# Kernel optimization log

Hardware: AMD Instinct MI355X
Metric: run time of the kernel (lower is better)

## Reference

```python
import jax, jax.numpy as jnp
import numpy as np

B, N, D = 2, 2048, 1024
H, DH = 16, 64
EPS = 1e-5


def _layernorm(t, g, b):
    m = jnp.mean(t, axis=-1, keepdims=True)
    v = jnp.mean(jnp.square(t - m), axis=-1, keepdims=True)
    return (t - m) * jax.lax.rsqrt(v + EPS) * g + b


def setup_inputs() -> dict:
    key = jax.random.key(0)
    ks = jax.random.split(key, 4)
    return {
        "x": jax.random.normal(ks[0], (B, N, D), dtype=jnp.float32),
        "ln_g": jnp.ones((D,), jnp.float32),
        "ln_b": jnp.zeros((D,), jnp.float32),
        "lnc_g": jnp.ones((D,), jnp.float32),
        "lnc_b": jnp.zeros((D,), jnp.float32),
        "Wq": jax.random.normal(ks[1], (D, H * DH), jnp.float32) * 0.02,
        "Wkv": jax.random.normal(ks[2], (D, 2 * H * DH), jnp.float32) * 0.02,
        "Wo": jax.random.normal(ks[3], (H * DH, D), jnp.float32) * 0.02,
    }


def reference(x, ln_g, ln_b, lnc_g, lnc_b, Wq, Wkv, Wo):
    scale = DH ** (-0.5)
    xn = _layernorm(x, ln_g, ln_b)          # self-attn: context = x
    cn = _layernorm(x, lnc_g, lnc_b)
    q = xn @ Wq                              # [b, n, h*d]
    kv = cn @ Wkv
    k, v = jnp.split(kv, 2, axis=-1)
    # b n (h d) -> b h n d
    q = q.reshape(B, N, H, DH).transpose(0, 2, 1, 3)
    k = k.reshape(B, N, H, DH).transpose(0, 2, 1, 3)
    v = v.reshape(B, N, H, DH).transpose(0, 2, 1, 3)
    sim = jnp.einsum("bhnd,bhmd->bhnm", q, k) * scale
    neg = -jnp.finfo(sim.dtype).max
    causal = jnp.tril(jnp.ones((N, N), dtype=bool))  # allow j <= i
    sim = jnp.where(causal[None, None], sim, neg)
    attn = jax.nn.softmax(sim.astype(jnp.float32), axis=-1)
    out = jnp.einsum("bhnm,bhmd->bhnd", attn, v)
    out = out.transpose(0, 2, 1, 3).reshape(B, N, H * DH)
    return out @ Wo
```

## Files before the change

### kernel.cpp

```cpp
#include <hip/hip_runtime.h>
#include <hip/hip_bf16.h>

#define B_  2
#define N_  2048
#define D_  1024
#define H_  16
#define DH_ 64
#define BN_ROWS (B_ * N_)
#define EPS_ 1e-5f
#define QKV_N 3072

typedef __attribute__((ext_vector_type(8))) short bf16x8_t;
typedef __attribute__((ext_vector_type(4))) short bf16x4_t;
typedef __attribute__((ext_vector_type(4))) float f32x4_t;

#define MFMA16(a, b, c) __builtin_amdgcn_mfma_f32_16x16x16bf16_1k(a, b, c, 0, 0, 0)

typedef const unsigned int __attribute__((address_space(1)))* gas_ptr;
typedef unsigned int __attribute__((address_space(3)))* las_ptr;

__device__ __forceinline__ void async16(const unsigned short* g, unsigned short* l) {
    __builtin_amdgcn_global_load_lds((gas_ptr)g, (las_ptr)l, 16, 0, 0);
}

__device__ __forceinline__ unsigned short f2bf(float f) {
    unsigned int u = __float_as_uint(f);
    unsigned int r = u + 0x7FFFu + ((u >> 16) & 1u);
    return (unsigned short)(r >> 16);
}

__device__ __forceinline__ unsigned int pk2bf(float a, float b) {
    __hip_bfloat162 t = __float22bfloat162_rn(float2{a, b});
    return *(unsigned int*)&t;
}

__global__ __launch_bounds__(256) void ln_wt_kernel(
    const float* __restrict__ x,
    const float* __restrict__ g1, const float* __restrict__ b1,
    const float* __restrict__ g2, const float* __restrict__ b2,
    const float* __restrict__ Wq, const float* __restrict__ Wkv,
    const float* __restrict__ Wo,
    unsigned short* __restrict__ xn, unsigned short* __restrict__ cn,
    unsigned short* __restrict__ wqkvT, unsigned short* __restrict__ woT) {
    const int bid = blockIdx.x;
    const int tid = threadIdx.x;

    if (bid < BN_ROWS) {
        const int row = bid;
        const float4 v = ((const float4*)(x + (size_t)row * D_))[tid];

        float s  = v.x + v.y + v.z + v.w;
        float s2 = v.x * v.x + v.y * v.y + v.z * v.z + v.w * v.w;
        #pragma unroll
        for (int off = 32; off > 0; off >>= 1) {
            s  += __shfl_down(s,  off);
            s2 += __shfl_down(s2, off);
        }
        __shared__ float red[8];
        if ((tid & 63) == 0) { red[tid >> 6] = s; red[4 + (tid >> 6)] = s2; }
        __syncthreads();
        const float S  = red[0] + red[1] + red[2] + red[3];
        const float S2 = red[4] + red[5] + red[6] + red[7];
        const float mean = S * (1.0f / D_);
        const float var  = S2 * (1.0f / D_) - mean * mean;
        const float rstd = rsqrtf(var + EPS_);

        const float4 G1 = ((const float4*)g1)[tid];
        const float4 B1 = ((const float4*)b1)[tid];
        const float4 G2 = ((const float4*)g2)[tid];
        const float4 B2 = ((const float4*)b2)[tid];

        float nx[4] = { (v.x - mean) * rstd, (v.y - mean) * rstd,
                        (v.z - mean) * rstd, (v.w - mean) * rstd };
        ushort4 o1, o2;
        o1.x = f2bf(nx[0] * G1.x + B1.x); o1.y = f2bf(nx[1] * G1.y + B1.y);
        o1.z = f2bf(nx[2] * G1.z + B1.z); o1.w = f2bf(nx[3] * G1.w + B1.w);
        o2.x = f2bf(nx[0] * G2.x + B2.x); o2.y = f2bf(nx[1] * G2.y + B2.y);
        o2.z = f2bf(nx[2] * G2.z + B2.z); o2.w = f2bf(nx[3] * G2.w + B2.w);
        ((ushort4*)(xn + (size_t)row * D_))[tid] = o1;
        ((ushort4*)(cn + (size_t)row * D_))[tid] = o2;
    } else {
        const int zz = bid - BN_ROWS;
        const float* src;
        unsigned short* dst;
        int N, t;
        if (zz < 1024)      { src = Wq;  dst = wqkvT;                       N = 1024; t = zz; }
        else if (zz < 3072) { src = Wkv; dst = wqkvT + (size_t)1024 * 1024; N = 2048; t = zz - 1024; }
        else                { src = Wo;  dst = woT;                         N = 1024; t = zz - 3072; }
        const int nb = N / 32;
        const int n0 = (t % nb) * 32, k0 = (t / nb) * 32;

        __shared__ float tile[32][33];
        const int tx = tid & 31, ty = tid >> 5;
        #pragma unroll
        for (int i = 0; i < 4; i++)
            tile[ty + i * 8][tx] = src[(size_t)(k0 + ty + i * 8) * N + n0 + tx];
        __syncthreads();
        #pragma unroll
        for (int i = 0; i < 4; i++)
            dst[(size_t)(n0 + ty + i * 8) * 1024 + k0 + tx] = f2bf(tile[tx][ty + i * 8]);
    }
}

template <int BM, bool FUSED, bool BF16OUT, int MINW>
__global__ __launch_bounds__(256, MINW) void gemm_kernel(
    const unsigned short* __restrict__ A0, const unsigned short* __restrict__ A1,
    const unsigned short* __restrict__ Bt, void* __restrict__ Cv,
    unsigned short* __restrict__ vt, int M, int N, int K) {
    constexpr int WM = BM / 2, MT = WM / 16, AI = BM / 32;
    __shared__ unsigned short As[BM * 64];
    __shared__ unsigned short Bs[128 * 64];
    const int tid = threadIdx.x, lane = tid & 63, w = tid >> 6;
    const int quad = lane >> 4, l16 = lane & 15;
    const int lr8 = lane >> 3, pg8 = lane & 7;
    const int wr = (w >> 1) * WM, wc = (w & 1) * 64;
    const int bm = blockIdx.y * BM, bn = blockIdx.x * 128;
    const unsigned short* A = (FUSED && bn >= 1024) ? A1 : A0;
    const float cscale = (FUSED && bn < 1024) ? 0.180336880111120f : 1.0f;

    f32x4_t acc[MT][4] = {};
    for (int k0 = 0; k0 < K; k0 += 64) {
        #pragma unroll
        for (int i = 0; i < AI; i++) {
            const int rb = w * (BM / 4) + i * 8;
            const int r  = rb + lr8;
            const int g  = pg8 ^ (r & 7);
            async16(&A[(size_t)(bm + r) * K + k0 + g * 8], &As[rb * 64]);
        }
        #pragma unroll
        for (int i = 0; i < 4; i++) {
            const int rb = w * 32 + i * 8;
            const int r  = rb + lr8;
            const int g  = pg8 ^ (r & 7);
            async16(&Bt[(size_t)(bn + r) * K + k0 + g * 8], &Bs[rb * 64]);
        }
        __syncthreads();
        #pragma unroll
        for (int kk = 0; kk < 64; kk += 32) {
            bf16x8_t af[MT], bfr[4];
            const int g0 = (kk >> 3) + quad;
            #pragma unroll
            for (int t = 0; t < MT; t++)
                af[t] = *(const bf16x8_t*)&As[(wr + t * 16 + l16) * 64 +
                                              ((g0 ^ (l16 & 7)) * 8)];
            #pragma unroll
            for (int t = 0; t < 4; t++)
                bfr[t] = *(const bf16x8_t*)&Bs[(wc + t * 16 + l16) * 64 +
                                               ((g0 ^ (l16 & 7)) * 8)];
            #pragma unroll
            for (int mt = 0; mt < MT; mt++)
                #pragma unroll
                for (int nt = 0; nt < 4; nt++)
                    acc[mt][nt] = __builtin_amdgcn_mfma_f32_16x16x32_bf16(
                        af[mt], bfr[nt], acc[mt][nt], 0, 0, 0);
        }
        __syncthreads();
    }

    if (FUSED && bn >= 2048) {
        const int seq0 = bm + wr;
        const int bq = seq0 >> 11;
        const int kt = (seq0 & (N_ - 1)) >> 6;
        #pragma unroll
        for (int nt = 0; nt < 4; nt++) {
            const int c = (bn - 2048) + wc + nt * 16 + l16;
            unsigned short* dst =
                vt + (((size_t)(bq * 32 + kt) * 1024) + c) * 64;
            #pragma unroll
            for (int mt = 0; mt < 4; mt++) {
                uint2 v2 = { pk2bf(acc[mt][nt][0], acc[mt][nt][1]),
                             pk2bf(acc[mt][nt][2], acc[mt][nt][3]) };
                *(uint2*)&dst[mt * 16 + quad * 4] = v2;
            }
        }
        return;
    }

    #pragma unroll
    for (int mt = 0; mt < MT; mt++)
        #pragma unroll
        for (int nt = 0; nt < 4; nt++)
            #pragma unroll
            for (int r = 0; r < 4; r++) {
                const int row = bm + wr + mt * 16 + quad * 4 + r;
                const int col = bn + wc + nt * 16 + l16;
                if (BF16OUT)
                    ((unsigned short*)Cv)[(size_t)row * N + col] =
                        f2bf(acc[mt][nt][r] * cscale);
                else
                    ((float*)Cv)[(size_t)row * N + col] = acc[mt][nt][r];
            }
}

__global__ __launch_bounds__(512, 4) void flash_attn_kernel(
    const unsigned short* __restrict__ qkv, const unsigned short* __restrict__ vt,
    unsigned short* __restrict__ out) {
    __shared__ unsigned short Qs[64 * 64];
    __shared__ unsigned short Ks[2][64 * 64];
    __shared__ unsigned short Vts[3][64 * 64];

    const int tid = threadIdx.x, lane = tid & 63, w = tid >> 6;
    const int quad = lane >> 4, l16 = lane & 15;
    const int lr8 = lane >> 3, pg8 = lane & 7;
    const int wq = w & 3;
    const int wk = w >> 2;
    const int bid = blockIdx.x;
    const int bh   = (bid & 7) * 4 + ((bid >> 3) & 3);
    const int pair = bid >> 5;
    const int b = bh >> 4, h = bh & 15;

    const unsigned short* qb  = qkv + (size_t)(b * N_) * QKV_N + h * DH_;
    const unsigned short* kb  = qb + 1024;
    const unsigned short* vtb = vt + ((size_t)(b * 32) * 1024 + h * 64) * 64;

    bf16x4_t ones4;
    #pragma unroll
    for (int j = 0; j < 4; j++) ones4[j] = (short)0x3F80;

    for (int phase = 0; phase < 2; phase++) {
        const int qt = phase ? (31 - pair) : pair;
        const int qs = qt * 64;
        const int niter = qt + 1;

        __syncthreads();

        f32x4_t o[4] = {};
        f32x4_t lacc = {};
        bf16x8_t qf[2];
        bf16x4_t pf[2];

        auto prefetch = [&](int t) {
            const int ksel = t & 1, vsel = t % 3;
            const int rb = w * 8;
            const int r  = rb + lr8;
            const int g  = pg8 ^ (r & 7);
            async16(&kb[(size_t)(t * 64 + r) * QKV_N + g * 8], &Ks[ksel][rb * 64]);
            async16(&vtb[((size_t)t * 1024 + r) * 64 + g * 8], &Vts[vsel][rb * 64]);
        };
        auto do_qk = [&](int kbuf, f32x4_t* s) {
            #pragma unroll
            for (int k2 = 0; k2 < 2; k2++) {
                const int g0 = k2 * 4 + quad;
                #pragma unroll
                for (int kt = 0; kt < 2; kt++) {
                    const int ktg = wk * 2 + kt;
                    const bf16x8_t a = *(const bf16x8_t*)&Ks[kbuf][
                        (ktg * 16 + l16) * 64 + (g0 ^ (l16 & 7)) * 8];
                    s[kt] = __builtin_amdgcn_mfma_f32_16x16x32_bf16(
                        a, qf[k2], s[kt], 0, 0, 0);
                }
            }
        };
        auto do_exp = [&](const f32x4_t* s, int js, bool edge) {
            #pragma unroll
            for (int kt = 0; kt < 2; kt++) {
                const int ktg = wk * 2 + kt;
                float p[4];
                #pragma unroll
                for (int r = 0; r < 4; r++) {
                    float sv = s[kt][r];
                    if (edge) {
                        const int key = js + ktg * 16 + quad * 4 + r;
                        const int qy  = qs + wq * 16 + l16;
                        if (key > qy) sv = -3e38f;
                    }
                    p[r] = __builtin_amdgcn_exp2f(sv);
                }
                uint2 pk = { pk2bf(p[0], p[1]), pk2bf(p[2], p[3]) };
                pf[kt] = *(bf16x4_t*)&pk;
            }
        };
        auto do_pv = [&](int vbuf) {
            #pragma unroll
            for (int kt = 0; kt < 2; kt++) {
                const int ktg = wk * 2 + kt;
                const int g = ktg * 2 + (quad >> 1);
                const int col = ((g ^ (l16 & 7)) * 8) + (quad & 1) * 4;
                #pragma unroll
                for (int nt = 0; nt < 4; nt++) {
                    const bf16x4_t bv = *(const bf16x4_t*)&Vts[vbuf][
                        (nt * 16 + l16) * 64 + col];
                    o[nt] = MFMA16(pf[kt], bv, o[nt]);
                }
                lacc = MFMA16(pf[kt], ones4, lacc);
            }
        };

        {
            const int rb = w * 8;
            const int r  = rb + lr8;
            const int g  = pg8 ^ (r & 7);
            async16(&qb[(size_t)(qs + r) * QKV_N + g * 8], &Qs[rb * 64]);
        }
        prefetch(0);
        __syncthreads();

        if (niter > 1) prefetch(1);
        #pragma unroll
        for (int k2 = 0; k2 < 2; k2++) {
            const int g0 = k2 * 4 + quad;
            qf[k2] = *(const bf16x8_t*)&Qs[
                (wq * 16 + l16) * 64 + (g0 ^ (l16 & 7)) * 8];
        }
        {
            f32x4_t s[2] = {};
            do_qk(0, s);
            do_exp(s, 0, niter == 1);
        }

        for (int jt = 1; jt < niter; jt++) {
            __syncthreads();
            if (jt + 1 < niter) prefetch(jt + 1);
            f32x4_t s[2] = {};
            do_qk(jt & 1, s);
            do_pv((jt - 1) % 3);
            do_exp(s, jt * 64, jt == niter - 1);
        }
        do_pv((niter - 1) % 3);

        __syncthreads();
        float* red = (float*)&Vts[0][0];
        if (wk == 1) {
            #pragma unroll
            for (int r = 0; r < 4; r++) {
                const int q = quad * 4 + r;
                const int base = (wq * 16 + q) * 68;
                #pragma unroll
                for (int nt = 0; nt < 4; nt++)
                    red[base + nt * 16 + l16] = o[nt][r];
                red[base + 64] = lacc[r];
            }
        }
        __syncthreads();
        if (wk == 0) {
            #pragma unroll
            for (int r = 0; r < 4; r++) {
                const int q = quad * 4 + r;
                const int base = (wq * 16 + q) * 68;
                #pragma unroll
                for (int nt = 0; nt < 4; nt++)
                    o[nt][r] += red[base + nt * 16 + l16];
                const float inv = 1.0f / (lacc[r] + red[base + 64]);
                const int query = qs + wq * 16 + quad * 4 + r;
                const int row = b * N_ + query;
                #pragma unroll
                for (int nt = 0; nt < 4; nt++) {
                    const int col = h * DH_ + nt * 16 + l16;
                    out[(size_t)row * (H_ * DH_) + col] = f2bf(o[nt][r] * inv);
                }
            }
        }
    }
}

extern "C" void kernel_launch(void* const* d_in, const int* in_sizes, int n_in,
                              void* d_out, int out_size, void* d_ws, size_t ws_size,
                              hipStream_t stream) {
    const float* x     = (const float*)d_in[0];
    const float* ln_g  = (const float*)d_in[1];
    const float* ln_b  = (const float*)d_in[2];
    const float* lnc_g = (const float*)d_in[3];
    const float* lnc_b = (const float*)d_in[4];
    const float* Wq    = (const float*)d_in[5];
    const float* Wkv   = (const float*)d_in[6];
    const float* Wo    = (const float*)d_in[7];

    char* ws = (char*)d_ws;
    const size_t MB = 1024 * 1024;
    unsigned short* qkv   = (unsigned short*)(ws + 0 * MB);
    unsigned short* vtbuf = (unsigned short*)(ws + 24 * MB);
    unsigned short* xn    = (unsigned short*)(ws + 32 * MB);
    unsigned short* cn    = (unsigned short*)(ws + 40 * MB);
    unsigned short* wqkvT = (unsigned short*)(ws + 48 * MB);
    unsigned short* woT   = (unsigned short*)(ws + 54 * MB);
    unsigned short* ao    = xn;

    ln_wt_kernel<<<8192, 256, 0, stream>>>(
        x, ln_g, ln_b, lnc_g, lnc_b, Wq, Wkv, Wo, xn, cn, wqkvT, woT);

    gemm_kernel<128, true, true, 3>
        <<<dim3(QKV_N / 128, BN_ROWS / 128), 256, 0, stream>>>(
        xn, cn, wqkvT, qkv, vtbuf, BN_ROWS, QKV_N, D_);

    flash_attn_kernel<<<B_ * H_ * 16, 512, 0, stream>>>(qkv, vtbuf, ao);

    gemm_kernel<64, false, false, 2>
        <<<dim3(D_ / 128, BN_ROWS / 64), 256, 0, stream>>>(
        ao, nullptr, woT, (float*)d_out, nullptr, BN_ROWS, D_, H_ * DH_);
}
```

Measured before the change: 175.7 us.

## Load Q and K fragments directly to registers and repartition attention warps

The flash attention kernel no longer stages Q and K through LDS. Each wave loads its Q fragments (two 16-row tiles) and a 16-key slice of K straight from global memory into registers, double-buffered across iterations, while V is still staged asynchronously in LDS. Work is split so each wave owns one 16-key slice and 32 query rows, and the four partial accumulators are merged by a two-level LDS tree reduction. This cuts LDS traffic and capacity, but adds uncoalesced global loads for K, more accumulator registers, and extra barriers in the epilogue.

```diff
diff --git a/kernel.cpp b/kernel.cpp
--- a/kernel.cpp
+++ b/kernel.cpp
@@ -15,6 +15,7 @@
 typedef __attribute__((ext_vector_type(4))) float f32x4_t;
 
 #define MFMA16(a, b, c) __builtin_amdgcn_mfma_f32_16x16x16bf16_1k(a, b, c, 0, 0, 0)
+#define MFMA32(a, b, c) __builtin_amdgcn_mfma_f32_16x16x32_bf16(a, b, c, 0, 0, 0)
 
 typedef const unsigned int __attribute__((address_space(1)))* gas_ptr;
 typedef unsigned int __attribute__((address_space(3)))* las_ptr;
@@ -151,8 +152,7 @@
             for (int mt = 0; mt < MT; mt++)
                 #pragma unroll
                 for (int nt = 0; nt < 4; nt++)
-                    acc[mt][nt] = __builtin_amdgcn_mfma_f32_16x16x32_bf16(
-                        af[mt], bfr[nt], acc[mt][nt], 0, 0, 0);
+                    acc[mt][nt] = MFMA32(af[mt], bfr[nt], acc[mt][nt]);
         }
         __syncthreads();
     }
@@ -195,15 +195,14 @@
 __global__ __launch_bounds__(512, 4) void flash_attn_kernel(
     const unsigned short* __restrict__ qkv, const unsigned short* __restrict__ vt,
     unsigned short* __restrict__ out) {
-    __shared__ unsigned short Qs[64 * 64];
-    __shared__ unsigned short Ks[2][64 * 64];
     __shared__ unsigned short Vts[3][64 * 64];
+    __shared__ float Red[2 * 64 * 66];
 
     const int tid = threadIdx.x, lane = tid & 63, w = tid >> 6;
     const int quad = lane >> 4, l16 = lane & 15;
     const int lr8 = lane >> 3, pg8 = lane & 7;
-    const int wq = w & 3;
-    const int wk = w >> 2;
+    const int kt  = w & 3;
+    const int qth = w >> 2;
     const int bid = blockIdx.x;
     const int bh   = (bid & 7) * 4 + ((bid >> 3) & 3);
     const int pair = bid >> 5;
@@ -218,137 +217,165 @@
     for (int j = 0; j < 4; j++) ones4[j] = (short)0x3F80;
 
     for (int phase = 0; phase < 2; phase++) {
-        const int qt = phase ? (31 - pair) : pair;
-        const int qs = qt * 64;
-        const int niter = qt + 1;
-
-        __syncthreads();
-
-        f32x4_t o[4] = {};
-        f32x4_t lacc = {};
-        bf16x8_t qf[2];
-        bf16x4_t pf[2];
-
-        auto prefetch = [&](int t) {
-            const int ksel = t & 1, vsel = t % 3;
-            const int rb = w * 8;
-            const int r  = rb + lr8;
-            const int g  = pg8 ^ (r & 7);
-            async16(&kb[(size_t)(t * 64 + r) * QKV_N + g * 8], &Ks[ksel][rb * 64]);
-            async16(&vtb[((size_t)t * 1024 + r) * 64 + g * 8], &Vts[vsel][rb * 64]);
+        const int qti = phase ? (31 - pair) : pair;
+        const int qs = qti * 64;
+        const int niter = qti + 1;
+
+        f32x4_t o[2][4] = {};
+        f32x4_t lacc[2] = {};
+        bf16x8_t qf[2][2];
+        bf16x4_t pfA[2];
+        bf16x8_t k0r[2], k1r[2];
+
+        auto stageV = [&](int t) {
+            const int vsel = t % 3;
+            const int r = w * 8 + lr8;
+            const int g = pg8 ^ (r & 7);
+            async16(&vtb[((size_t)t * 1024 + r) * 64 + g * 8],
+                    &Vts[vsel][(w * 8) * 64]);
         };
-        auto do_qk = [&](int kbuf, f32x4_t* s) {
-            #pragma unroll
-            for (int k2 = 0; k2 < 2; k2++) {
-                const int g0 = k2 * 4 + quad;
-                #pragma unroll
-                for (int kt = 0; kt < 2; kt++) {
-                    const int ktg = wk * 2 + kt;
-                    const bf16x8_t a = *(const bf16x8_t*)&Ks[kbuf][
-                        (ktg * 16 + l16) * 64 + (g0 ^ (l16 & 7)) * 8];
-                    s[kt] = __builtin_amdgcn_mfma_f32_16x16x32_bf16(
-                        a, qf[k2], s[kt], 0, 0, 0);
-                }
-            }
+        auto loadK = [&](int t, bf16x8_t (&kr)[2]) {
+            #pragma unroll
+            for (int k2 = 0; k2 < 2; k2++)
+                kr[k2] = *(const bf16x8_t*)&kb[
+                    (size_t)(t * 64 + kt * 16 + l16) * QKV_N + (k2 * 4 + quad) * 8];
+        };
+        auto do_qk = [&](const bf16x8_t (&kr)[2], f32x4_t* s) {
+            #pragma unroll
+            for (int k2 = 0; k2 < 2; k2++)
+                #pragma unroll
+                for (int qt = 0; qt < 2; qt++)
+                    s[qt] = MFMA32(kr[k2], qf[qt][k2], s[qt]);
         };
         auto do_exp = [&](const f32x4_t* s, int js, bool edge) {
             #pragma unroll
-            for (int kt = 0; kt < 2; kt++) {
-                const int ktg = wk * 2 + kt;
+            for (int qt = 0; qt < 2; qt++) {
                 float p[4];
                 #pragma unroll
                 for (int r = 0; r < 4; r++) {
-                    float sv = s[kt][r];
+                    float sv = s[qt][r];
                     if (edge) {
-                        const int key = js + ktg * 16 + quad * 4 + r;
-                        const int qy  = qs + wq * 16 + l16;
+                        const int key = js + kt * 16 + quad * 4 + r;
+                        const int qy  = qs + qth * 32 + qt * 16 + l16;
                         if (key > qy) sv = -3e38f;
                     }
                     p[r] = __builtin_amdgcn_exp2f(sv);
                 }
                 uint2 pk = { pk2bf(p[0], p[1]), pk2bf(p[2], p[3]) };
-                pf[kt] = *(bf16x4_t*)&pk;
+                pfA[qt] = *(bf16x4_t*)&pk;
             }
         };
         auto do_pv = [&](int vbuf) {
-            #pragma unroll
-            for (int kt = 0; kt < 2; kt++) {
-                const int ktg = wk * 2 + kt;
-                const int g = ktg * 2 + (quad >> 1);
-                const int col = ((g ^ (l16 & 7)) * 8) + (quad & 1) * 4;
-                #pragma unroll
-                for (int nt = 0; nt < 4; nt++) {
-                    const bf16x4_t bv = *(const bf16x4_t*)&Vts[vbuf][
-                        (nt * 16 + l16) * 64 + col];
-                    o[nt] = MFMA16(pf[kt], bv, o[nt]);
-                }
-                lacc = MFMA16(pf[kt], ones4, lacc);
+            const int col = (((kt * 2 + (quad >> 1)) ^ (l16 & 7)) * 8)
+                            + (quad & 1) * 4;
+            #pragma unroll
+            for (int nt = 0; nt < 4; nt++) {
+                const bf16x4_t bv = *(const bf16x4_t*)&Vts[vbuf][
+                    (nt * 16 + l16) * 64 + col];
+                #pragma unroll
+                for (int qt = 0; qt < 2; qt++)
+                    o[qt][nt] = MFMA16(pfA[qt], bv, o[qt][nt]);
             }
+            #pragma unroll
+            for (int qt = 0; qt < 2; qt++)
+                lacc[qt] = MFMA16(pfA[qt], ones4, lacc[qt]);
         };
 
-        {
-            const int rb = w * 8;
-            const int r  = rb + lr8;
-            const int g  = pg8 ^ (r & 7);
-            async16(&qb[(size_t)(qs + r) * QKV_N + g * 8], &Qs[rb * 64]);
-        }
-        prefetch(0);
-        __syncthreads();
-
-        if (niter > 1) prefetch(1);
-        #pragma unroll
-        for (int k2 = 0; k2 < 2; k2++) {
-            const int g0 = k2 * 4 + quad;
-            qf[k2] = *(const bf16x8_t*)&Qs[
-                (wq * 16 + l16) * 64 + (g0 ^ (l16 & 7)) * 8];
-        }
+        #pragma unroll
+        for (int qt = 0; qt < 2; qt++)
+            #pragma unroll
+            for (int k2 = 0; k2 < 2; k2++)
+                qf[qt][k2] = *(const bf16x8_t*)&qb[
+                    (size_t)(qs + qth * 32 + qt * 16 + l16) * QKV_N
+                    + (k2 * 4 + quad) * 8];
+        stageV(0);
+        loadK(0, k0r);
+        __syncthreads();
+        if (niter > 1) { stageV(1); loadK(1, k1r); }
         {
             f32x4_t s[2] = {};
-            do_qk(0, s);
+            do_qk(k0r, s);
             do_exp(s, 0, niter == 1);
         }
 
         for (int jt = 1; jt < niter; jt++) {
             __syncthreads();
-            if (jt + 1 < niter) prefetch(jt + 1);
+            const bool nxt = (jt + 1 < niter);
             f32x4_t s[2] = {};
-            do_qk(jt & 1, s);
+            if (jt & 1) {
+                if (nxt) { stageV(jt + 1); loadK(jt + 1, k0r); }
+                do_qk(k1r, s);
+            } else {
+                if (nxt) { stageV(jt + 1); loadK(jt + 1, k1r); }
+                do_qk(k0r, s);
+            }
             do_pv((jt - 1) % 3);
             do_exp(s, jt * 64, jt == niter - 1);
         }
         do_pv((niter - 1) % 3);
 
-        __syncthreads();
-        float* red = (float*)&Vts[0][0];
-        if (wk == 1) {
-            #pragma unroll
-            for (int r = 0; r < 4; r++) {
-                const int q = quad * 4 + r;
-                const int base = (wq * 16 + q) * 68;
-                #pragma unroll
-                for (int nt = 0; nt < 4; nt++)
-                    red[base + nt * 16 + l16] = o[nt][r];
-                red[base + 64] = lacc[r];
-            }
-        }
-        __syncthreads();
-        if (wk == 0) {
-            #pragma unroll
-            for (int r = 0; r < 4; r++) {
-                const int q = quad * 4 + r;
-                const int base = (wq * 16 + q) * 68;
-                #pragma unroll
-                for (int nt = 0; nt < 4; nt++)
-                    o[nt][r] += red[base + nt * 16 + l16];
-                const float inv = 1.0f / (lacc[r] + red[base + 64]);
-                const int query = qs + wq * 16 + quad * 4 + r;
-                const int row = b * N_ + query;
-                #pragma unroll
-                for (int nt = 0; nt < 4; nt++) {
-                    const int col = h * DH_ + nt * 16 + l16;
-                    out[(size_t)row * (H_ * DH_) + col] = f2bf(o[nt][r] * inv);
+        if (kt & 1) {
+            float* R = &Red[(kt >> 1) * 64 * 66];
+            #pragma unroll
+            for (int qt = 0; qt < 2; qt++)
+                #pragma unroll
+                for (int r = 0; r < 4; r++) {
+                    const int row = qth * 32 + qt * 16 + quad * 4 + r;
+                    #pragma unroll
+                    for (int nt = 0; nt < 4; nt++)
+                        R[row * 66 + nt * 16 + l16] = o[qt][nt][r];
+                    R[row * 66 + 64] = lacc[qt][r];
                 }
-            }
+        }
+        __syncthreads();
+        if (!(kt & 1)) {
+            float* R = &Red[(kt >> 1) * 64 * 66];
+            #pragma unroll
+            for (int qt = 0; qt < 2; qt++)
+                #pragma unroll
+                for (int r = 0; r < 4; r++) {
+                    const int row = qth * 32 + qt * 16 + quad * 4 + r;
+                    #pragma unroll
+                    for (int nt = 0; nt < 4; nt++)
+                        o[qt][nt][r] += R[row * 66 + nt * 16 + l16];
+                    lacc[qt][r] += R[row * 66 + 64];
+                }
+        }
+        __syncthreads();
+        if (kt == 2) {
+            float* R = &Red[0];
+            #pragma unroll
+            for (int qt = 0; qt < 2; qt++)
+                #pragma unroll
+                for (int r = 0; r < 4; r++) {
+                    const int row = qth * 32 + qt * 16 + quad * 4 + r;
+                    #pragma unroll
+                    for (int nt = 0; nt < 4; nt++)
+                        R[row * 66 + nt * 16 + l16] = o[qt][nt][r];
+                    R[row * 66 + 64] = lacc[qt][r];
+                }
+        }
+        __syncthreads();
+        if (kt == 0) {
+            float* R = &Red[0];
+            #pragma unroll
+            for (int qt = 0; qt < 2; qt++)
+                #pragma unroll
+                for (int r = 0; r < 4; r++) {
+                    const int row = qth * 32 + qt * 16 + quad * 4 + r;
+                    #pragma unroll
+                    for (int nt = 0; nt < 4; nt++)
+                        o[qt][nt][r] += R[row * 66 + nt * 16 + l16];
+                    const float inv = 1.0f / (lacc[qt][r] + R[row * 66 + 64]);
+                    const int query = qs + row;
+                    const int orow  = b * N_ + query;
+                    #pragma unroll
+                    for (int nt = 0; nt < 4; nt++) {
+                        const int col = h * DH_ + nt * 16 + l16;
+                        out[(size_t)orow * (H_ * DH_) + col] =
+                            f2bf(o[qt][nt][r] * inv);
+                    }
+                }
         }
     }
 }
```

Measured after the change: 197.5 us. 1.12x slower.
